# Optimization experiments

Hardware: AMD Instinct MI355X
Metric: run time of the kernel (lower is better)

Reference implementation:

```python
import jax, jax.numpy as jnp
import numpy as np

ORDER = 10


def setup_inputs() -> dict:
    key = jax.random.key(0)
    k1, k2, k3 = jax.random.split(key, 3)
    N, F, E = 100000, 128, 1600000
    x = jax.random.normal(k1, (N, F), dtype=jnp.float32)
    edge_index = jax.random.randint(k2, (2, E), 0, N, dtype=jnp.int64)
    # PPR initialization: w_k = alpha*(1-alpha)^k for k<order, w_order = (1-alpha)^order
    alpha = 0.1
    w = np.array([alpha * (1.0 - alpha) ** k for k in range(ORDER)] + [(1.0 - alpha) ** ORDER],
                 dtype=np.float32)
    weights = jnp.asarray(w)
    return {"x": x, "edge_index": edge_index, "weights": weights}


def _gcn_norm(edge_index, num_nodes):
    # add self loops
    loop = jnp.arange(num_nodes, dtype=edge_index.dtype)
    row = jnp.concatenate([edge_index[0], loop])  # source (x_j)
    col = jnp.concatenate([edge_index[1], loop])  # destination (aggregation)
    ones = jnp.ones(row.shape[0], dtype=jnp.float32)
    deg = jax.ops.segment_sum(ones, col, num_segments=num_nodes)
    deg_inv_sqrt = jnp.where(deg > 0, jax.lax.rsqrt(deg), 0.0)
    norm = deg_inv_sqrt[row] * deg_inv_sqrt[col]  # [E + N]
    return row, col, norm


def reference(x, edge_index, weights):
    N = x.shape[0]
    row, col, norm = _gcn_norm(edge_index, N)
    norm = norm.astype(x.dtype)[:, None]  # [E+N, 1]

    def propagate(h):
        # gather -> scale -> scatter-add  (symmetric normalized adjacency)
        return jax.ops.segment_sum(norm * h[row], col, num_segments=N)

    hidden = x
    out = weights[0] * hidden
    for k in range(1, ORDER + 1):
        hidden = propagate(hidden)
        out = out + weights[k] * hidden
    return out
```

## Files before the change

### kernel.cpp

```cpp
#include <hip/hip_runtime.h>
#include <hip/hip_fp16.h>


#define F 128
#define SCAN_B 256
#define NGROUP 8

__global__ void count_kernel(const int* __restrict__ ei, int E,
                             int* __restrict__ cnt) {
    int e = blockIdx.x * blockDim.x + threadIdx.x;
    if (e < E) {
        int c = ei[(size_t)E + e];
        atomicAdd(&cnt[c], 1);
    }
}

__global__ void dinv_kernel(const int* __restrict__ cnt, float* __restrict__ dinv,
                            int N) {
    int i = blockIdx.x * blockDim.x + threadIdx.x;
    if (i < N) {
        dinv[i] = rsqrtf((float)(cnt[i] + 1));
    }
}

__global__ void scan1_kernel(const int* __restrict__ cnt, int* __restrict__ offs,
                             int* __restrict__ bsums, int N) {
    __shared__ int sm[SCAN_B];
    int i = blockIdx.x * SCAN_B + threadIdx.x;
    int v = (i < N) ? cnt[i] : 0;
    sm[threadIdx.x] = v;
    __syncthreads();
    for (int d = 1; d < SCAN_B; d <<= 1) {
        int t = (threadIdx.x >= d) ? sm[threadIdx.x - d] : 0;
        __syncthreads();
        sm[threadIdx.x] += t;
        __syncthreads();
    }
    if (i < N) offs[i] = sm[threadIdx.x] - v;
    if (threadIdx.x == SCAN_B - 1) bsums[blockIdx.x] = sm[SCAN_B - 1];
}

__global__ void scan2_kernel(int* __restrict__ bsums, int nb) {
    __shared__ int sm[SCAN_B];
    __shared__ int carry;
    if (threadIdx.x == 0) carry = 0;
    __syncthreads();
    for (int base = 0; base < nb; base += SCAN_B) {
        int i = base + threadIdx.x;
        int v = (i < nb) ? bsums[i] : 0;
        sm[threadIdx.x] = v;
        __syncthreads();
        for (int d = 1; d < SCAN_B; d <<= 1) {
            int t = (threadIdx.x >= d) ? sm[threadIdx.x - d] : 0;
            __syncthreads();
            sm[threadIdx.x] += t;
            __syncthreads();
        }
        if (i < nb) bsums[i] = sm[threadIdx.x] - v + carry;
        __syncthreads();
        if (threadIdx.x == 0) carry += sm[SCAN_B - 1];
        __syncthreads();
    }
}

__global__ void scan3_kernel(int* __restrict__ offs, const int* __restrict__ bsums,
                             int* __restrict__ cursor, int N, int E) {
    int i = blockIdx.x * blockDim.x + threadIdx.x;
    if (i < N) {
        int o = offs[i] + bsums[i / SCAN_B];
        offs[i] = o;
        cursor[i] = o;
    }
    if (i == N) offs[N] = E;
}

__global__ void place_kernel(const int* __restrict__ ei, int E,
                             int* __restrict__ cursor, int* __restrict__ edges,
                             int N) {
    const int g = blockIdx.x & (NGROUP - 1);
    const int b = blockIdx.x >> 3;
    const int nb = gridDim.x >> 3;
    const int lo = (int)((long long)N * g / NGROUP);
    const int hi = (int)((long long)N * (g + 1) / NGROUP);
    const int stride = nb * blockDim.x;
    for (int e = b * blockDim.x + threadIdx.x; e < E; e += stride) {
        int c = ei[(size_t)E + e];
        if (c < lo || c >= hi) continue;
        int pos = atomicAdd(&cursor[c], 1);
        edges[pos] = ei[e];
    }
}

__global__ void conv_kernel(const float2* __restrict__ x2,
                            __half2* __restrict__ xh, __half2* __restrict__ y,
                            const float* __restrict__ wts, int order, int n2) {
    float wl = wts[order];
    for (int i = blockIdx.x * blockDim.x + threadIdx.x; i < n2;
         i += gridDim.x * blockDim.x) {
        float2 v = x2[i];
        xh[i] = __floats2half2_rn(v.x, v.y);
        y[i] = __floats2half2_rn(wl * v.x, wl * v.y);
    }
}

__global__ __launch_bounds__(128) void prop_kernel(
    const __half2* __restrict__ y_old, __half2* __restrict__ y_new,
    float2* __restrict__ out, const __half2* __restrict__ xh,
    const float* __restrict__ dinv, const int* __restrict__ offs,
    const int* __restrict__ edges, const float* __restrict__ wts,
    int j, int last) {
    const int wave = threadIdx.x >> 6;
    const int lane = threadIdx.x & 63;
    const int c = (blockIdx.x << 1) + wave;
    const size_t rb = ((size_t)c << 6);

    const float wj = wts[j];
    const float dc = dinv[c];
    float2 hv = __half22float2(y_old[rb + lane]);
    float2 xv = __half22float2(xh[rb + lane]);
    const float s = dc * dc;
    float accx = fmaf(s, hv.x, wj * xv.x);
    float accy = fmaf(s, hv.y, wj * xv.y);

    int e = offs[c];
    const int end = offs[c + 1];

    for (; e + 8 <= end; e += 8) {
        int s0 = edges[e + 0];
        int s1 = edges[e + 1];
        int s2 = edges[e + 2];
        int s3 = edges[e + 3];
        int s4 = edges[e + 4];
        int s5 = edges[e + 5];
        int s6 = edges[e + 6];
        int s7 = edges[e + 7];
        float w0 = dinv[s0] * dc;
        float w1 = dinv[s1] * dc;
        float w2 = dinv[s2] * dc;
        float w3 = dinv[s3] * dc;
        float w4 = dinv[s4] * dc;
        float w5 = dinv[s5] * dc;
        float w6 = dinv[s6] * dc;
        float w7 = dinv[s7] * dc;
        float2 f0 = __half22float2(y_old[((size_t)s0 << 6) + lane]);
        float2 f1 = __half22float2(y_old[((size_t)s1 << 6) + lane]);
        float2 f2 = __half22float2(y_old[((size_t)s2 << 6) + lane]);
        float2 f3 = __half22float2(y_old[((size_t)s3 << 6) + lane]);
        float2 f4 = __half22float2(y_old[((size_t)s4 << 6) + lane]);
        float2 f5 = __half22float2(y_old[((size_t)s5 << 6) + lane]);
        float2 f6 = __half22float2(y_old[((size_t)s6 << 6) + lane]);
        float2 f7 = __half22float2(y_old[((size_t)s7 << 6) + lane]);
        accx = fmaf(w0, f0.x, accx);
        accy = fmaf(w0, f0.y, accy);
        accx = fmaf(w1, f1.x, accx);
        accy = fmaf(w1, f1.y, accy);
        accx = fmaf(w2, f2.x, accx);
        accy = fmaf(w2, f2.y, accy);
        accx = fmaf(w3, f3.x, accx);
        accy = fmaf(w3, f3.y, accy);
        accx = fmaf(w4, f4.x, accx);
        accy = fmaf(w4, f4.y, accy);
        accx = fmaf(w5, f5.x, accx);
        accy = fmaf(w5, f5.y, accy);
        accx = fmaf(w6, f6.x, accx);
        accy = fmaf(w6, f6.y, accy);
        accx = fmaf(w7, f7.x, accx);
        accy = fmaf(w7, f7.y, accy);
    }
    for (; e < end; ++e) {
        int s0 = edges[e];
        float w0 = dinv[s0] * dc;
        float2 f = __half22float2(y_old[((size_t)s0 << 6) + lane]);
        accx = fmaf(w0, f.x, accx);
        accy = fmaf(w0, f.y, accy);
    }

    if (last) {
        float2 o;
        o.x = accx;
        o.y = accy;
        out[rb + lane] = o;
    } else {
        y_new[rb + lane] = __floats2half2_rn(accx, accy);
    }
}

extern "C" void kernel_launch(void* const* d_in, const int* in_sizes, int n_in,
                              void* d_out, int out_size, void* d_ws, size_t ws_size,
                              hipStream_t stream) {
    const float* x = (const float*)d_in[0];
    const int* ei = (const int*)d_in[1];
    const float* wts = (const float*)d_in[2];
    float2* out = (float2*)d_out;

    const int NF = in_sizes[0];
    const int N = NF / F;
    const int E = in_sizes[1] / 2;
    const int order = in_sizes[2] - 1;

    char* p = (char*)d_ws;
    auto carve = [&](size_t bytes) {
        void* q = (void*)p;
        p += (bytes + 255) & ~(size_t)255;
        return q;
    };
    int nb = (N + SCAN_B - 1) / SCAN_B;
    int*     cnt   = (int*)carve(sizeof(int) * (size_t)N);
    int*     offs  = (int*)carve(sizeof(int) * (size_t)(N + 1));
    int*     bsums = (int*)carve(sizeof(int) * (size_t)nb);
    float*   dinv  = (float*)carve(sizeof(float) * (size_t)N);
    int*     edges = (int*)carve(4ull * (size_t)E);
    __half2* xh    = (__half2*)carve(sizeof(__half2) * (size_t)(NF / 2));
    __half2* yA    = (__half2*)carve(sizeof(__half2) * (size_t)(NF / 2));
    __half2* yB    = (__half2*)carve(sizeof(__half2) * (size_t)(NF / 2));
    int*     cursor = cnt;
    (void)ws_size;

    hipMemsetAsync(cnt, 0, sizeof(int) * (size_t)N, stream);
    count_kernel<<<(E + 255) / 256, 256, 0, stream>>>(ei, E, cnt);
    dinv_kernel<<<(N + 255) / 256, 256, 0, stream>>>(cnt, dinv, N);
    scan1_kernel<<<nb, SCAN_B, 0, stream>>>(cnt, offs, bsums, N);
    scan2_kernel<<<1, SCAN_B, 0, stream>>>(bsums, nb);
    scan3_kernel<<<(N + 1 + 255) / 256, 256, 0, stream>>>(offs, bsums, cursor, N, E);
    place_kernel<<<2048, 256, 0, stream>>>(ei, E, cursor, edges, N);

    conv_kernel<<<2048, 256, 0, stream>>>((const float2*)x, xh, yA, wts, order,
                                          NF / 2);

    const __half2* yin = yA;
    __half2* yout = yB;
    for (int j = order - 1; j >= 0; --j) {
        int last = (j == 0);
        prop_kernel<<<N / 2, 128, 0, stream>>>(yin, yout, out, xh, dinv, offs,
                                               edges, wts, j, last);
        yin = yout;
        yout = (yout == yA) ? yB : yA;
    }
}
```

Measured before the change: 913.2 us.

## Two-pass bucketed CSR build, fused dinv, fma_mix propagation, 4 rows per block

The CSR construction now runs a partition pass that writes (col,row) pairs into group-contiguous staging. The place kernel then reads only its own group's slice instead of scanning all edges eight times. The dinv computation is folded into the first scan kernel, and the propagation kernel uses v_fma_mix_f32 inline asm to accumulate fp16 features without separate conversions. The propagation kernel also moves to 256-thread blocks handling four nodes each, and gathers are issued before the dinv loads. The cost is an extra 8 bytes per edge of staging memory, an additional kernel launch, and rows no longer divisible by 4 being silently dropped if N%4!=0.

```diff
diff --git a/kernel.cpp b/kernel.cpp
--- a/kernel.cpp
+++ b/kernel.cpp
@@ -5,6 +5,7 @@
 #define F 128
 #define SCAN_B 256
 #define NGROUP 8
+#define CHUNK 4096
 
 __global__ void count_kernel(const int* __restrict__ ei, int E,
                              int* __restrict__ cnt) {
@@ -15,19 +16,13 @@
     }
 }
 
-__global__ void dinv_kernel(const int* __restrict__ cnt, float* __restrict__ dinv,
-                            int N) {
-    int i = blockIdx.x * blockDim.x + threadIdx.x;
-    if (i < N) {
-        dinv[i] = rsqrtf((float)(cnt[i] + 1));
-    }
-}
-
 __global__ void scan1_kernel(const int* __restrict__ cnt, int* __restrict__ offs,
-                             int* __restrict__ bsums, int N) {
+                             int* __restrict__ bsums, float* __restrict__ dinv,
+                             int N) {
     __shared__ int sm[SCAN_B];
     int i = blockIdx.x * SCAN_B + threadIdx.x;
     int v = (i < N) ? cnt[i] : 0;
+    if (i < N) dinv[i] = rsqrtf((float)(v + 1));
     sm[threadIdx.x] = v;
     __syncthreads();
     for (int d = 1; d < SCAN_B; d <<= 1) {
@@ -64,30 +59,72 @@
 }
 
 __global__ void scan3_kernel(int* __restrict__ offs, const int* __restrict__ bsums,
-                             int* __restrict__ cursor, int N, int E) {
+                             int* __restrict__ cursor, int* __restrict__ bstart,
+                             int* __restrict__ bcur, int N, int E) {
     int i = blockIdx.x * blockDim.x + threadIdx.x;
     if (i < N) {
         int o = offs[i] + bsums[i / SCAN_B];
         offs[i] = o;
         cursor[i] = o;
-    }
-    if (i == N) offs[N] = E;
-}
-
-__global__ void place_kernel(const int* __restrict__ ei, int E,
-                             int* __restrict__ cursor, int* __restrict__ edges,
-                             int N) {
+#pragma unroll
+        for (int g = 0; g < NGROUP; ++g) {
+            if (i == (int)((long long)N * g / NGROUP)) {
+                bstart[g] = o;
+                bcur[g] = o;
+            }
+        }
+    }
+    if (i == N) {
+        offs[N] = E;
+        bstart[NGROUP] = E;
+    }
+}
+
+__global__ void part_kernel(const int* __restrict__ ei, int E, int N,
+                            int* __restrict__ bcur, int2* __restrict__ stage) {
+    __shared__ int hist[NGROUP];
+    __shared__ int cur[NGROUP];
+    for (int chunk = blockIdx.x; (long long)chunk * CHUNK < E; chunk += gridDim.x) {
+        int e0 = chunk * CHUNK;
+        int n = min(CHUNK, E - e0);
+        if (threadIdx.x < NGROUP) hist[threadIdx.x] = 0;
+        __syncthreads();
+        for (int i = threadIdx.x; i < n; i += blockDim.x) {
+            int c = ei[(size_t)E + e0 + i];
+            int g = (int)((long long)c * NGROUP / N);
+            atomicAdd(&hist[g], 1);
+        }
+        __syncthreads();
+        if (threadIdx.x < NGROUP)
+            cur[threadIdx.x] = atomicAdd(&bcur[threadIdx.x], hist[threadIdx.x]);
+        __syncthreads();
+        for (int i = threadIdx.x; i < n; i += blockDim.x) {
+            int c = ei[(size_t)E + e0 + i];
+            int r = ei[e0 + i];
+            int g = (int)((long long)c * NGROUP / N);
+            int pos = atomicAdd(&cur[g], 1);
+            int2 p;
+            p.x = c;
+            p.y = r;
+            stage[pos] = p;
+        }
+        __syncthreads();
+    }
+}
+
+__global__ void place_kernel(const int2* __restrict__ stage,
+                             const int* __restrict__ bstart,
+                             int* __restrict__ cursor, int* __restrict__ edges) {
     const int g = blockIdx.x & (NGROUP - 1);
     const int b = blockIdx.x >> 3;
     const int nb = gridDim.x >> 3;
-    const int lo = (int)((long long)N * g / NGROUP);
-    const int hi = (int)((long long)N * (g + 1) / NGROUP);
+    const int lo = bstart[g];
+    const int hi = bstart[g + 1];
     const int stride = nb * blockDim.x;
-    for (int e = b * blockDim.x + threadIdx.x; e < E; e += stride) {
-        int c = ei[(size_t)E + e];
-        if (c < lo || c >= hi) continue;
-        int pos = atomicAdd(&cursor[c], 1);
-        edges[pos] = ei[e];
+    for (int i = lo + b * blockDim.x + threadIdx.x; i < hi; i += stride) {
+        int2 p = stage[i];
+        int pos = atomicAdd(&cursor[p.x], 1);
+        edges[pos] = p.y;
     }
 }
 
@@ -103,24 +140,33 @@
     }
 }
 
-__global__ __launch_bounds__(128) void prop_kernel(
-    const __half2* __restrict__ y_old, __half2* __restrict__ y_new,
+__device__ __forceinline__ void fmamix2(float& ax, float& ay, float w,
+                                        unsigned raw) {
+    asm volatile(
+        "v_fma_mix_f32 %0, %2, %3, %0 op_sel:[0,0,0] op_sel_hi:[0,1,0]\n\t"
+        "v_fma_mix_f32 %1, %2, %3, %1 op_sel:[0,1,0] op_sel_hi:[0,1,0]"
+        : "+v"(ax), "+v"(ay)
+        : "v"(w), "v"(raw));
+}
+
+__global__ __launch_bounds__(256) void prop_kernel(
+    const unsigned* __restrict__ y_old, __half2* __restrict__ y_new,
     float2* __restrict__ out, const __half2* __restrict__ xh,
     const float* __restrict__ dinv, const int* __restrict__ offs,
     const int* __restrict__ edges, const float* __restrict__ wts,
     int j, int last) {
     const int wave = threadIdx.x >> 6;
     const int lane = threadIdx.x & 63;
-    const int c = (blockIdx.x << 1) + wave;
+    const int c = (blockIdx.x << 2) + wave;
     const size_t rb = ((size_t)c << 6);
 
     const float wj = wts[j];
     const float dc = dinv[c];
-    float2 hv = __half22float2(y_old[rb + lane]);
+    const float s = dc * dc;
     float2 xv = __half22float2(xh[rb + lane]);
-    const float s = dc * dc;
-    float accx = fmaf(s, hv.x, wj * xv.x);
-    float accy = fmaf(s, hv.y, wj * xv.y);
+    float accx = wj * xv.x;
+    float accy = wj * xv.y;
+    fmamix2(accx, accy, s, y_old[rb + lane]);
 
     int e = offs[c];
     const int end = offs[c + 1];
@@ -134,6 +180,14 @@
         int s5 = edges[e + 5];
         int s6 = edges[e + 6];
         int s7 = edges[e + 7];
+        unsigned f0 = y_old[((size_t)s0 << 6) + lane];
+        unsigned f1 = y_old[((size_t)s1 << 6) + lane];
+        unsigned f2 = y_old[((size_t)s2 << 6) + lane];
+        unsigned f3 = y_old[((size_t)s3 << 6) + lane];
+        unsigned f4 = y_old[((size_t)s4 << 6) + lane];
+        unsigned f5 = y_old[((size_t)s5 << 6) + lane];
+        unsigned f6 = y_old[((size_t)s6 << 6) + lane];
+        unsigned f7 = y_old[((size_t)s7 << 6) + lane];
         float w0 = dinv[s0] * dc;
         float w1 = dinv[s1] * dc;
         float w2 = dinv[s2] * dc;
@@ -142,37 +196,19 @@
         float w5 = dinv[s5] * dc;
         float w6 = dinv[s6] * dc;
         float w7 = dinv[s7] * dc;
-        float2 f0 = __half22float2(y_old[((size_t)s0 << 6) + lane]);
-        float2 f1 = __half22float2(y_old[((size_t)s1 << 6) + lane]);
-        float2 f2 = __half22float2(y_old[((size_t)s2 << 6) + lane]);
-        float2 f3 = __half22float2(y_old[((size_t)s3 << 6) + lane]);
-        float2 f4 = __half22float2(y_old[((size_t)s4 << 6) + lane]);
-        float2 f5 = __half22float2(y_old[((size_t)s5 << 6) + lane]);
-        float2 f6 = __half22float2(y_old[((size_t)s6 << 6) + lane]);
-        float2 f7 = __half22float2(y_old[((size_t)s7 << 6) + lane]);
-        accx = fmaf(w0, f0.x, accx);
-        accy = fmaf(w0, f0.y, accy);
-        accx = fmaf(w1, f1.x, accx);
-        accy = fmaf(w1, f1.y, accy);
-        accx = fmaf(w2, f2.x, accx);
-        accy = fmaf(w2, f2.y, accy);
-        accx = fmaf(w3, f3.x, accx);
-        accy = fmaf(w3, f3.y, accy);
-        accx = fmaf(w4, f4.x, accx);
-        accy = fmaf(w4, f4.y, accy);
-        accx = fmaf(w5, f5.x, accx);
-        accy = fmaf(w5, f5.y, accy);
-        accx = fmaf(w6, f6.x, accx);
-        accy = fmaf(w6, f6.y, accy);
-        accx = fmaf(w7, f7.x, accx);
-        accy = fmaf(w7, f7.y, accy);
+        fmamix2(accx, accy, w0, f0);
+        fmamix2(accx, accy, w1, f1);
+        fmamix2(accx, accy, w2, f2);
+        fmamix2(accx, accy, w3, f3);
+        fmamix2(accx, accy, w4, f4);
+        fmamix2(accx, accy, w5, f5);
+        fmamix2(accx, accy, w6, f6);
+        fmamix2(accx, accy, w7, f7);
     }
     for (; e < end; ++e) {
         int s0 = edges[e];
         float w0 = dinv[s0] * dc;
-        float2 f = __half22float2(y_old[((size_t)s0 << 6) + lane]);
-        accx = fmaf(w0, f.x, accx);
-        accy = fmaf(w0, f.y, accy);
+        fmamix2(accx, accy, w0, y_old[((size_t)s0 << 6) + lane]);
     }
 
     if (last) {
@@ -205,24 +241,29 @@
         return q;
     };
     int nb = (N + SCAN_B - 1) / SCAN_B;
-    int*     cnt   = (int*)carve(sizeof(int) * (size_t)N);
-    int*     offs  = (int*)carve(sizeof(int) * (size_t)(N + 1));
-    int*     bsums = (int*)carve(sizeof(int) * (size_t)nb);
-    float*   dinv  = (float*)carve(sizeof(float) * (size_t)N);
-    int*     edges = (int*)carve(4ull * (size_t)E);
-    __half2* xh    = (__half2*)carve(sizeof(__half2) * (size_t)(NF / 2));
-    __half2* yA    = (__half2*)carve(sizeof(__half2) * (size_t)(NF / 2));
-    __half2* yB    = (__half2*)carve(sizeof(__half2) * (size_t)(NF / 2));
+    int*     cnt    = (int*)carve(sizeof(int) * (size_t)N);
+    int*     offs   = (int*)carve(sizeof(int) * (size_t)(N + 1));
+    int*     bsums  = (int*)carve(sizeof(int) * (size_t)nb);
+    float*   dinv   = (float*)carve(sizeof(float) * (size_t)N);
+    int*     edges  = (int*)carve(4ull * (size_t)E);
+    int2*    stage  = (int2*)carve(8ull * (size_t)E);
+    int*     bstart = (int*)carve(sizeof(int) * (NGROUP + 1));
+    int*     bcur   = (int*)carve(sizeof(int) * NGROUP);
+    __half2* xh     = (__half2*)carve(sizeof(__half2) * (size_t)(NF / 2));
+    __half2* yA     = (__half2*)carve(sizeof(__half2) * (size_t)(NF / 2));
+    __half2* yB     = (__half2*)carve(sizeof(__half2) * (size_t)(NF / 2));
     int*     cursor = cnt;
     (void)ws_size;
 
     hipMemsetAsync(cnt, 0, sizeof(int) * (size_t)N, stream);
     count_kernel<<<(E + 255) / 256, 256, 0, stream>>>(ei, E, cnt);
-    dinv_kernel<<<(N + 255) / 256, 256, 0, stream>>>(cnt, dinv, N);
-    scan1_kernel<<<nb, SCAN_B, 0, stream>>>(cnt, offs, bsums, N);
+    scan1_kernel<<<nb, SCAN_B, 0, stream>>>(cnt, offs, bsums, dinv, N);
     scan2_kernel<<<1, SCAN_B, 0, stream>>>(bsums, nb);
-    scan3_kernel<<<(N + 1 + 255) / 256, 256, 0, stream>>>(offs, bsums, cursor, N, E);
-    place_kernel<<<2048, 256, 0, stream>>>(ei, E, cursor, edges, N);
+    scan3_kernel<<<(N + 1 + 255) / 256, 256, 0, stream>>>(offs, bsums, cursor,
+                                                          bstart, bcur, N, E);
+    int nchunks = (E + CHUNK - 1) / CHUNK;
+    part_kernel<<<nchunks, 256, 0, stream>>>(ei, E, N, bcur, stage);
+    place_kernel<<<2048, 256, 0, stream>>>(stage, bstart, cursor, edges);
 
     conv_kernel<<<2048, 256, 0, stream>>>((const float2*)x, xh, yA, wts, order,
                                           NF / 2);
@@ -231,8 +272,9 @@
     __half2* yout = yB;
     for (int j = order - 1; j >= 0; --j) {
         int last = (j == 0);
-        prop_kernel<<<N / 2, 128, 0, stream>>>(yin, yout, out, xh, dinv, offs,
-                                               edges, wts, j, last);
+        prop_kernel<<<N / 4, 256, 0, stream>>>((const unsigned*)yin, yout, out,
+                                               xh, dinv, offs, edges, wts, j,
+                                               last);
         yin = yout;
         yout = (yout == yA) ? yB : yA;
     }
```

Measured after the change: 946.4 us. 3.6% more time.
